# Kernel tuning notes

Measured on AMD Instinct MI355X. Metric: run time of the kernel, lower is better.

Reference implementation:

```python
import jax, jax.numpy as jnp
import numpy as np

HEADS = 16

def _rope(x):
    # x: (B, H, T, D); rotate pairs (even, odd) along last dim, positions along axis 2
    B, H, T, D = x.shape
    half = D // 2
    theta = 10000.0 ** (-jnp.arange(half, dtype=x.dtype) / half)          # (half,)
    angles = jnp.arange(T, dtype=x.dtype)[:, None] * theta                # (T, half)
    sin, cos = jnp.sin(angles), jnp.cos(angles)                           # (T, half)
    x1, x2 = x[..., ::2], x[..., 1::2]                                    # (B,H,T,half)
    rot = jnp.stack([x1 * cos - x2 * sin, x1 * sin + x2 * cos], axis=-1)  # (B,H,T,half,2)
    return rot.reshape(B, H, T, D)

def setup_inputs() -> dict:
    key = jax.random.key(0)
    k1, k2, k3 = jax.random.split(key, 3)
    B, T, C = 2, 2048, 1024
    return {
        "x": jax.random.normal(k1, (B, T, C), dtype=jnp.float32),
        "W_qkv": jax.random.normal(k2, (3 * C, C), dtype=jnp.float32) * 0.02,
        "W_out": jax.random.normal(k3, (C, C), dtype=jnp.float32) * 0.02,
        "window": 256,
    }

def reference(x, W_qkv, W_out, window):
    B, T, C = x.shape
    H = HEADS
    D = C // H
    # fused QKV projection (torch Linear: y = x @ W.T)
    qkv = jnp.einsum('btc,fc->btf', x, W_qkv)            # (B,T,3C)
    qkv = qkv.reshape(B, T, H, 3 * D).transpose(0, 2, 1, 3)  # (B,H,T,3D)
    q, k, v = jnp.split(qkv, 3, axis=-1)                 # each (B,H,T,D)
    q, k = _rope(q), _rope(k)
    # causal + local-window boolean mask: allow j in [i-window, i]
    i = jnp.arange(T)[:, None]
    j = jnp.arange(T)[None, :]
    mask = (j <= i) & (j >= i - window)                  # (T,T) bool
    scale = 1.0 / jnp.sqrt(jnp.asarray(D, dtype=x.dtype))
    scores = jnp.einsum('bhqd,bhkd->bhqk', q, k) * scale # (B,H,T,T)
    scores = jnp.where(mask[None, None], scores, -jnp.inf)
    attn = jax.nn.softmax(scores, axis=-1)
    out = jnp.einsum('bhqk,bhkd->bhqd', attn, v)         # (B,H,T,D)
    out = out.transpose(0, 2, 1, 3).reshape(B, T, C)
    return jnp.einsum('btc,oc->bto', out, W_out)
```

## Files before the change

kernel.cpp:

```cpp
#include <hip/hip_runtime.h>

typedef float f32x4 __attribute__((ext_vector_type(4)));
typedef __bf16 bf16x8 __attribute__((ext_vector_type(8)));
typedef unsigned short u16x4 __attribute__((ext_vector_type(4)));

__device__ __forceinline__ unsigned short f2bf(float f) {
  union { float f; unsigned int u; } v; v.f = f;
  unsigned int r = (v.u + 0x7FFFu + ((v.u >> 16) & 1u)) >> 16;
  return (unsigned short)r;
}
__device__ __forceinline__ float bf2f(unsigned short h) {
  union { unsigned int u; float f; } v; v.u = ((unsigned int)h) << 16;
  return v.f;
}
__device__ __forceinline__ void gload_lds16(const void* g, void* l) {
  __builtin_amdgcn_global_load_lds(
      (const __attribute__((address_space(1))) unsigned int*)g,
      (__attribute__((address_space(3))) unsigned int*)l, 16, 0, 0);
}

__global__ __launch_bounds__(256) void prep_kernel(
    const float* __restrict__ x, const float* __restrict__ wqkv,
    const float* __restrict__ wout, unsigned short* __restrict__ xb,
    unsigned short* __restrict__ wqkvb, unsigned short* __restrict__ woutb,
    float2* __restrict__ tab) {
  const int N1 = 1048576, N2 = 786432, N3 = 262144;
  int idx = blockIdx.x * 256 + threadIdx.x;
  if (idx < N1 + N2 + N3) {
    const float* src; unsigned short* dst; int i = idx;
    if (i < N1)           { src = x;    dst = xb; }
    else if (i < N1 + N2) { i -= N1;      src = wqkv; dst = wqkvb; }
    else                  { i -= N1 + N2; src = wout; dst = woutb; }
    float4 v = ((const float4*)src)[i];
    u16x4 o;
    o.x = f2bf(v.x); o.y = f2bf(v.y); o.z = f2bf(v.z); o.w = f2bf(v.w);
    ((u16x4*)dst)[i] = o;
  } else {
    int i = idx - (N1 + N2 + N3);
    if (i < 65536) {
      int t = i >> 5, p = i & 31;
      float theta = exp2f(-(float)p * 0.4152410118609203f);
      float sn, cs;
      sincosf((float)t * theta, &sn, &cs);
      tab[i] = make_float2(cs, sn);
    }
  }
}

#define G1_SLOT ((128 + 256) * 64)

__global__ __launch_bounds__(512, 1) void gemm1_qkv(
    const unsigned short* __restrict__ A,
    const unsigned short* __restrict__ B,
    unsigned short* __restrict__ Cq,
    const float2* __restrict__ tab) {
  __shared__ unsigned short lds[3 * G1_SLOT];
  const int K = 1024, NJ = 3072, NT = 16;
  const int tid = threadIdx.x;
  const int bm = blockIdx.y * 128, bn = blockIdx.x * 256;
  const int lane = tid & 63, w = tid >> 6, wr = w >> 2, wc = w & 3;
  const int rq = lane & 15, hi = lane >> 4;

  auto stage = [&](int slot, int kt) {
    unsigned short* s = lds + slot * G1_SLOT;
#pragma unroll
    for (int p = 0; p < 2; ++p) {
      int ch = tid + p * 512;
      int row = ch >> 3, blk = (ch & 7) ^ (row & 7);
      gload_lds16(A + (size_t)(bm + row) * K + kt + blk * 8, s + ch * 8);
    }
#pragma unroll
    for (int p = 0; p < 4; ++p) {
      int ch = tid + p * 512;
      int row = ch >> 3, blk = (ch & 7) ^ (row & 7);
      gload_lds16(B + (size_t)(bn + row) * K + kt + blk * 8,
                  s + 128 * 64 + ch * 8);
    }
  };

  f32x4 acc[4][4] = {};
  auto compute = [&](int slot) {
    const unsigned short* sA = lds + slot * G1_SLOT;
    const unsigned short* sB = sA + 128 * 64;
#pragma unroll
    for (int k = 0; k < 2; ++k) {
      bf16x8 fa[4], fb[4];
#pragma unroll
      for (int m = 0; m < 4; ++m) {
        int r = wr * 64 + m * 16 + rq;
        int b = (hi + k * 4) ^ (r & 7);
        fa[m] = *(const bf16x8*)(sA + r * 64 + b * 8);
      }
#pragma unroll
      for (int n = 0; n < 4; ++n) {
        int r = wc * 64 + n * 16 + rq;
        int b = (hi + k * 4) ^ (r & 7);
        fb[n] = *(const bf16x8*)(sB + r * 64 + b * 8);
      }
#pragma unroll
      for (int m = 0; m < 4; ++m)
#pragma unroll
        for (int n = 0; n < 4; ++n)
          acc[m][n] = __builtin_amdgcn_mfma_f32_16x16x32_bf16(fa[m], fb[n], acc[m][n], 0, 0, 0);
    }
  };

  stage(0, 0);
  stage(1, 64);
  for (int t = 0; t < NT; ++t) {
    asm volatile("s_waitcnt lgkmcnt(0)" ::: "memory");
    __builtin_amdgcn_s_barrier();
    if (t + 2 < NT) stage((t + 2) % 3, (t + 2) * 64);
    if (t < NT - 2)
      asm volatile("s_waitcnt vmcnt(12)" ::: "memory");
    else if (t == NT - 2)
      asm volatile("s_waitcnt vmcnt(6)" ::: "memory");
    else
      asm volatile("s_waitcnt vmcnt(0)" ::: "memory");
    __builtin_amdgcn_s_barrier();
    compute(t % 3);
  }

  const int r0 = bm + wr * 64 + hi * 4;
  const int c0 = bn + wc * 64 + rq;
#pragma unroll
  for (int m = 0; m < 4; ++m)
#pragma unroll
    for (int n = 0; n < 4; ++n) {
      int col = c0 + n * 16;
      int cw = col % 192;
      bool dorot = cw < 128;
      int p = (cw & 63) >> 1;
#pragma unroll
      for (int j = 0; j < 4; ++j) {
        int row = r0 + m * 16 + j;
        float val = acc[m][n][j];
        float part = __shfl_xor(val, 1);
        float outv = val;
        if (dorot) {
          float2 cssn = tab[(row & 2047) * 32 + p];
          outv = (col & 1) ? (part * cssn.y + val * cssn.x)
                           : (val * cssn.x - part * cssn.y);
        }
        Cq[(size_t)row * NJ + col] = f2bf(outv);
      }
    }
}

template <bool OUTBF16>
__global__ __launch_bounds__(256) void gemm_bt(const unsigned short* __restrict__ A,
                                               const unsigned short* __restrict__ B,
                                               void* __restrict__ C,
                                               int M, int N, int K) {
  __shared__ unsigned short As[128][32];
  __shared__ unsigned short Bs[128][32];
  const int tid = threadIdx.x;
  const int lane = tid & 63;
  const int w = tid >> 6, wr = w >> 1, wc = w & 1;
  const int bm = blockIdx.y * 128, bn = blockIdx.x * 128;
  const int t4 = tid >> 2, c8 = (tid & 3) * 8;
  const unsigned short* Ab = A + (size_t)(bm + t4) * K + c8;
  const unsigned short* Bb = B + (size_t)(bn + t4) * K + c8;
  const int rq = lane & 15, kg = (lane >> 4) * 8;
  f32x4 acc[4][4] = {};
  for (int kt = 0; kt < K; kt += 32) {
    gload_lds16(Ab + kt,                  &As[t4][c8]);
    gload_lds16(Ab + kt + (size_t)64 * K, &As[t4 + 64][c8]);
    gload_lds16(Bb + kt,                  &Bs[t4][c8]);
    gload_lds16(Bb + kt + (size_t)64 * K, &Bs[t4 + 64][c8]);
    __syncthreads();
    bf16x8 fa[4], fb[4];
#pragma unroll
    for (int m = 0; m < 4; ++m) fa[m] = *(const bf16x8*)&As[wr * 64 + m * 16 + rq][kg];
#pragma unroll
    for (int n = 0; n < 4; ++n) fb[n] = *(const bf16x8*)&Bs[wc * 64 + n * 16 + rq][kg];
#pragma unroll
    for (int m = 0; m < 4; ++m)
#pragma unroll
      for (int n = 0; n < 4; ++n)
        acc[m][n] = __builtin_amdgcn_mfma_f32_16x16x32_bf16(fa[m], fb[n], acc[m][n], 0, 0, 0);
    __syncthreads();
  }
  const int r0 = bm + wr * 64 + (lane >> 4) * 4;
  const int c0 = bn + wc * 64 + rq;
#pragma unroll
  for (int m = 0; m < 4; ++m)
#pragma unroll
    for (int n = 0; n < 4; ++n)
#pragma unroll
      for (int j = 0; j < 4; ++j) {
        int row = r0 + m * 16 + j, col = c0 + n * 16;
        if (OUTBF16)
          ((unsigned short*)C)[(size_t)row * N + col] = f2bf(acc[m][n][j]);
        else
          ((float*)C)[(size_t)row * N + col] = acc[m][n][j];
      }
}

#define WMAX 256
__global__ __launch_bounds__(256) void attn_kernel(const unsigned short* __restrict__ qkv,
                                                   unsigned short* __restrict__ attnb,
                                                   const int* __restrict__ winp) {
  __shared__ unsigned short Qs[64][72];
  __shared__ unsigned short KPs[320 * 72];
  __shared__ unsigned short Vt[64][328];
  const int T = 2048;
  const int tid = threadIdx.x;
  const int bid = blockIdx.x;
  const int qt = bid & 31;
  const int bh = bid >> 5;
  const int b = bh >> 4, h = bh & 15;
  const int qbase = qt * 64;
  const int kbase = qbase - WMAX;
  const int win = *winp;
  const unsigned short* base = qkv + (size_t)b * T * 3072 + h * 192;
  const int tr = tid >> 2, tc = (tid & 3) * 16;
  {
    const unsigned short* s = base + (size_t)(qbase + tr) * 3072 + tc;
    *(int4*)&Qs[tr][tc]     = *(const int4*)s;
    *(int4*)&Qs[tr][tc + 8] = *(const int4*)(s + 8);
  }
#pragma unroll
  for (int p5 = 0; p5 < 5; ++p5) {
    int s = p5 * 64 + tr;
    int j = kbase + s;
    int jc = j < 0 ? 0 : j;
    const unsigned short* sk = base + (size_t)jc * 3072 + 64 + tc;
    *(int4*)&KPs[s * 72 + tc]     = *(const int4*)sk;
    *(int4*)&KPs[s * 72 + tc + 8] = *(const int4*)(sk + 8);
    const unsigned short* sv = base + (size_t)jc * 3072 + 128 + tc;
    unsigned short tmp[16];
    *(int4*)&tmp[0] = *(const int4*)sv;
    *(int4*)&tmp[8] = *(const int4*)(sv + 8);
#pragma unroll
    for (int e = 0; e < 16; ++e) Vt[tc + e][s] = tmp[e];
  }
  __syncthreads();
  const int lane = tid & 63, wv = tid >> 6;
  const int rbase = wv * 16;
  const int rq = lane & 15, kg = (lane >> 4) * 8;
  bf16x8 qa[2];
#pragma unroll
  for (int kk = 0; kk < 2; ++kk)
    qa[kk] = *(const bf16x8*)&Qs[rbase + rq][kk * 32 + kg];
  float sc[20][4];
#pragma unroll
  for (int n = 0; n < 20; ++n) {
    f32x4 s = {};
#pragma unroll
    for (int kk = 0; kk < 2; ++kk) {
      bf16x8 kb = *(const bf16x8*)&KPs[(n * 16 + rq) * 72 + kk * 32 + kg];
      s = __builtin_amdgcn_mfma_f32_16x16x32_bf16(qa[kk], kb, s, 0, 0, 0);
    }
#pragma unroll
    for (int r = 0; r < 4; ++r) sc[n][r] = s[r];
  }
  const float scale = 0.125f;
#pragma unroll
  for (int r = 0; r < 4; ++r) {
    const int i = qbase + rbase + (lane >> 4) * 4 + r;
    float mx = -1e30f;
#pragma unroll
    for (int n = 0; n < 20; ++n) {
      int j = kbase + n * 16 + rq;
      bool valid = (j >= 0) && (j <= i) && (i - j <= win);
      float v = valid ? sc[n][r] * scale : -1e30f;
      sc[n][r] = v;
      mx = fmaxf(mx, v);
    }
#pragma unroll
    for (int off = 1; off < 16; off <<= 1) mx = fmaxf(mx, __shfl_xor(mx, off));
    float sum = 0.f;
#pragma unroll
    for (int n = 0; n < 20; ++n) {
      float pv = __expf(sc[n][r] - mx);
      sc[n][r] = pv;
      sum += pv;
    }
#pragma unroll
    for (int off = 1; off < 16; off <<= 1) sum += __shfl_xor(sum, off);
    float inv = 1.0f / sum;
#pragma unroll
    for (int n = 0; n < 20; ++n) sc[n][r] *= inv;
  }
  __syncthreads();
#pragma unroll
  for (int n = 0; n < 20; ++n)
#pragma unroll
    for (int r = 0; r < 4; ++r)
      KPs[(rbase + (lane >> 4) * 4 + r) * 328 + n * 16 + rq] = f2bf(sc[n][r]);
  f32x4 oacc[4] = {};
#pragma unroll
  for (int kk = 0; kk < 10; ++kk) {
    bf16x8 pa = *(const bf16x8*)&KPs[(rbase + rq) * 328 + kk * 32 + kg];
#pragma unroll
    for (int n = 0; n < 4; ++n) {
      bf16x8 vb = *(const bf16x8*)&Vt[n * 16 + rq][kk * 32 + kg];
      oacc[n] = __builtin_amdgcn_mfma_f32_16x16x32_bf16(pa, vb, oacc[n], 0, 0, 0);
    }
  }
#pragma unroll
  for (int n = 0; n < 4; ++n)
#pragma unroll
    for (int j = 0; j < 4; ++j) {
      int r = qbase + rbase + (lane >> 4) * 4 + j;
      int d = n * 16 + rq;
      attnb[(size_t)(b * T + r) * 1024 + h * 64 + d] = f2bf(oacc[n][j]);
    }
}

extern "C" void kernel_launch(void* const* d_in, const int* in_sizes, int n_in,
                              void* d_out, int out_size, void* d_ws, size_t ws_size,
                              hipStream_t stream) {
  const float* x    = (const float*)d_in[0];
  const float* Wqkv = (const float*)d_in[1];
  const float* Wout = (const float*)d_in[2];
  const int*   winp = (const int*)d_in[3];

  const int M = 4096, C = 1024, N1 = 3072;
  unsigned short* xb    = (unsigned short*)d_ws;
  unsigned short* wqkvb = xb    + (size_t)M * C;
  unsigned short* woutb = wqkvb + (size_t)N1 * C;
  unsigned short* qkvb  = woutb + (size_t)C * C;
  unsigned short* attnb = qkvb  + (size_t)M * N1;
  float2*         tab   = (float2*)(attnb + (size_t)M * C);

  const int PREP = 1048576 + 786432 + 262144 + 65536;
  prep_kernel<<<(PREP + 255) / 256, 256, 0, stream>>>(x, Wqkv, Wout, xb, wqkvb,
                                                      woutb, tab);

  gemm1_qkv<<<dim3(12, 32), 512, 0, stream>>>(xb, wqkvb, qkvb, tab);

  attn_kernel<<<2 * 16 * 32, 256, 0, stream>>>(qkvb, attnb, winp);

  dim3 g2(C / 128, M / 128);
  gemm_bt<false><<<g2, 256, 0, stream>>>(attnb, woutb, (float*)d_out, M, C, C);
}
```

Measured before the change: 214.3 us.

## Simplify QKV GEMM to single-buffered tiles, swizzle V transpose, skip masked score tiles

The QKV projection GEMM drops its 512-thread, triple-buffered 128x256 pipeline and becomes the simpler 256-thread 128x128 single-stage loop, which raises block count but gives up load/compute overlap. The attention kernel now XOR-swizzles columns of the transposed V tile in shared memory to reduce bank conflicts. It also skips QK^T MFMAs for 16-key tiles that lie fully outside the causal range. The output GEMM template is reduced to a float-only version, which is a cleanup.

```diff
diff --git a/kernel.cpp b/kernel.cpp
--- a/kernel.cpp
+++ b/kernel.cpp
@@ -47,80 +47,41 @@
   }
 }
 
-#define G1_SLOT ((128 + 256) * 64)
-
-__global__ __launch_bounds__(512, 1) void gemm1_qkv(
+__global__ __launch_bounds__(256) void gemm1_rope(
     const unsigned short* __restrict__ A,
     const unsigned short* __restrict__ B,
     unsigned short* __restrict__ Cq,
     const float2* __restrict__ tab) {
-  __shared__ unsigned short lds[3 * G1_SLOT];
-  const int K = 1024, NJ = 3072, NT = 16;
+  __shared__ unsigned short As[128][32];
+  __shared__ unsigned short Bs[128][32];
+  const int K = 1024, NJ = 3072;
   const int tid = threadIdx.x;
-  const int bm = blockIdx.y * 128, bn = blockIdx.x * 256;
-  const int lane = tid & 63, w = tid >> 6, wr = w >> 2, wc = w & 3;
-  const int rq = lane & 15, hi = lane >> 4;
-
-  auto stage = [&](int slot, int kt) {
-    unsigned short* s = lds + slot * G1_SLOT;
-#pragma unroll
-    for (int p = 0; p < 2; ++p) {
-      int ch = tid + p * 512;
-      int row = ch >> 3, blk = (ch & 7) ^ (row & 7);
-      gload_lds16(A + (size_t)(bm + row) * K + kt + blk * 8, s + ch * 8);
-    }
-#pragma unroll
-    for (int p = 0; p < 4; ++p) {
-      int ch = tid + p * 512;
-      int row = ch >> 3, blk = (ch & 7) ^ (row & 7);
-      gload_lds16(B + (size_t)(bn + row) * K + kt + blk * 8,
-                  s + 128 * 64 + ch * 8);
-    }
-  };
-
+  const int lane = tid & 63;
+  const int w = tid >> 6, wr = w >> 1, wc = w & 1;
+  const int bm = blockIdx.y * 128, bn = blockIdx.x * 128;
+  const int t4 = tid >> 2, c8 = (tid & 3) * 8;
+  const unsigned short* Ab = A + (size_t)(bm + t4) * K + c8;
+  const unsigned short* Bb = B + (size_t)(bn + t4) * K + c8;
+  const int rq = lane & 15, hi = lane >> 4, kg = hi * 8;
   f32x4 acc[4][4] = {};
-  auto compute = [&](int slot) {
-    const unsigned short* sA = lds + slot * G1_SLOT;
-    const unsigned short* sB = sA + 128 * 64;
-#pragma unroll
-    for (int k = 0; k < 2; ++k) {
-      bf16x8 fa[4], fb[4];
-#pragma unroll
-      for (int m = 0; m < 4; ++m) {
-        int r = wr * 64 + m * 16 + rq;
-        int b = (hi + k * 4) ^ (r & 7);
-        fa[m] = *(const bf16x8*)(sA + r * 64 + b * 8);
-      }
-#pragma unroll
-      for (int n = 0; n < 4; ++n) {
-        int r = wc * 64 + n * 16 + rq;
-        int b = (hi + k * 4) ^ (r & 7);
-        fb[n] = *(const bf16x8*)(sB + r * 64 + b * 8);
-      }
-#pragma unroll
-      for (int m = 0; m < 4; ++m)
-#pragma unroll
-        for (int n = 0; n < 4; ++n)
-          acc[m][n] = __builtin_amdgcn_mfma_f32_16x16x32_bf16(fa[m], fb[n], acc[m][n], 0, 0, 0);
-    }
-  };
-
-  stage(0, 0);
-  stage(1, 64);
-  for (int t = 0; t < NT; ++t) {
-    asm volatile("s_waitcnt lgkmcnt(0)" ::: "memory");
-    __builtin_amdgcn_s_barrier();
-    if (t + 2 < NT) stage((t + 2) % 3, (t + 2) * 64);
-    if (t < NT - 2)
-      asm volatile("s_waitcnt vmcnt(12)" ::: "memory");
-    else if (t == NT - 2)
-      asm volatile("s_waitcnt vmcnt(6)" ::: "memory");
-    else
-      asm volatile("s_waitcnt vmcnt(0)" ::: "memory");
-    __builtin_amdgcn_s_barrier();
-    compute(t % 3);
-  }
-
+  for (int kt = 0; kt < K; kt += 32) {
+    gload_lds16(Ab + kt,                  &As[t4][c8]);
+    gload_lds16(Ab + kt + (size_t)64 * K, &As[t4 + 64][c8]);
+    gload_lds16(Bb + kt,                  &Bs[t4][c8]);
+    gload_lds16(Bb + kt + (size_t)64 * K, &Bs[t4 + 64][c8]);
+    __syncthreads();
+    bf16x8 fa[4], fb[4];
+#pragma unroll
+    for (int m = 0; m < 4; ++m) fa[m] = *(const bf16x8*)&As[wr * 64 + m * 16 + rq][kg];
+#pragma unroll
+    for (int n = 0; n < 4; ++n) fb[n] = *(const bf16x8*)&Bs[wc * 64 + n * 16 + rq][kg];
+#pragma unroll
+    for (int m = 0; m < 4; ++m)
+#pragma unroll
+      for (int n = 0; n < 4; ++n)
+        acc[m][n] = __builtin_amdgcn_mfma_f32_16x16x32_bf16(fa[m], fb[n], acc[m][n], 0, 0, 0);
+    __syncthreads();
+  }
   const int r0 = bm + wr * 64 + hi * 4;
   const int c0 = bn + wc * 64 + rq;
 #pragma unroll
@@ -147,11 +108,10 @@
     }
 }
 
-template <bool OUTBF16>
-__global__ __launch_bounds__(256) void gemm_bt(const unsigned short* __restrict__ A,
-                                               const unsigned short* __restrict__ B,
-                                               void* __restrict__ C,
-                                               int M, int N, int K) {
+__global__ __launch_bounds__(256) void gemm_bt_f32(const unsigned short* __restrict__ A,
+                                                   const unsigned short* __restrict__ B,
+                                                   float* __restrict__ C,
+                                                   int M, int N, int K) {
   __shared__ unsigned short As[128][32];
   __shared__ unsigned short Bs[128][32];
   const int tid = threadIdx.x;
@@ -188,13 +148,8 @@
 #pragma unroll
     for (int n = 0; n < 4; ++n)
 #pragma unroll
-      for (int j = 0; j < 4; ++j) {
-        int row = r0 + m * 16 + j, col = c0 + n * 16;
-        if (OUTBF16)
-          ((unsigned short*)C)[(size_t)row * N + col] = f2bf(acc[m][n][j]);
-        else
-          ((float*)C)[(size_t)row * N + col] = acc[m][n][j];
-      }
+      for (int j = 0; j < 4; ++j)
+        C[(size_t)(r0 + m * 16 + j) * N + c0 + n * 16] = acc[m][n][j];
 }
 
 #define WMAX 256
@@ -215,6 +170,7 @@
   const int win = *winp;
   const unsigned short* base = qkv + (size_t)b * T * 3072 + h * 192;
   const int tr = tid >> 2, tc = (tid & 3) * 16;
+  const int vswz = (tid & 3) << 4;
   {
     const unsigned short* s = base + (size_t)(qbase + tr) * 3072 + tc;
     *(int4*)&Qs[tr][tc]     = *(const int4*)s;
@@ -232,8 +188,9 @@
     unsigned short tmp[16];
     *(int4*)&tmp[0] = *(const int4*)sv;
     *(int4*)&tmp[8] = *(const int4*)(sv + 8);
-#pragma unroll
-    for (int e = 0; e < 16; ++e) Vt[tc + e][s] = tmp[e];
+    int ssw = s ^ vswz;
+#pragma unroll
+    for (int e = 0; e < 16; ++e) Vt[tc + e][ssw] = tmp[e];
   }
   __syncthreads();
   const int lane = tid & 63, wv = tid >> 6;
@@ -246,14 +203,20 @@
   float sc[20][4];
 #pragma unroll
   for (int n = 0; n < 20; ++n) {
-    f32x4 s = {};
-#pragma unroll
-    for (int kk = 0; kk < 2; ++kk) {
-      bf16x8 kb = *(const bf16x8*)&KPs[(n * 16 + rq) * 72 + kk * 32 + kg];
-      s = __builtin_amdgcn_mfma_f32_16x16x32_bf16(qa[kk], kb, s, 0, 0, 0);
-    }
-#pragma unroll
-    for (int r = 0; r < 4; ++r) sc[n][r] = s[r];
+    int jlo = kbase + n * 16;
+    if (jlo + 15 >= 0 && jlo <= qbase + rbase + 15) {
+      f32x4 s = {};
+#pragma unroll
+      for (int kk = 0; kk < 2; ++kk) {
+        bf16x8 kb = *(const bf16x8*)&KPs[(n * 16 + rq) * 72 + kk * 32 + kg];
+        s = __builtin_amdgcn_mfma_f32_16x16x32_bf16(qa[kk], kb, s, 0, 0, 0);
+      }
+#pragma unroll
+      for (int r = 0; r < 4; ++r) sc[n][r] = s[r];
+    } else {
+#pragma unroll
+      for (int r = 0; r < 4; ++r) sc[n][r] = -1e30f;
+    }
   }
   const float scale = 0.125f;
 #pragma unroll
@@ -295,7 +258,7 @@
     bf16x8 pa = *(const bf16x8*)&KPs[(rbase + rq) * 328 + kk * 32 + kg];
 #pragma unroll
     for (int n = 0; n < 4; ++n) {
-      bf16x8 vb = *(const bf16x8*)&Vt[n * 16 + rq][kk * 32 + kg];
+      bf16x8 vb = *(const bf16x8*)&Vt[n * 16 + rq][(kk * 32 + kg) ^ (n << 4)];
       oacc[n] = __builtin_amdgcn_mfma_f32_16x16x32_bf16(pa, vb, oacc[n], 0, 0, 0);
     }
   }
@@ -329,10 +292,10 @@
   prep_kernel<<<(PREP + 255) / 256, 256, 0, stream>>>(x, Wqkv, Wout, xb, wqkvb,
                                                       woutb, tab);
 
-  gemm1_qkv<<<dim3(12, 32), 512, 0, stream>>>(xb, wqkvb, qkvb, tab);
+  gemm1_rope<<<dim3(N1 / 128, M / 128), 256, 0, stream>>>(xb, wqkvb, qkvb, tab);
 
   attn_kernel<<<2 * 16 * 32, 256, 0, stream>>>(qkvb, attnb, winp);
 
-  dim3 g2(C / 128, M / 128);
-  gemm_bt<false><<<g2, 256, 0, stream>>>(attnb, woutb, (float*)d_out, M, C, C);
-}
+  gemm_bt_f32<<<dim3(C / 128, M / 128), 256, 0, stream>>>(attnb, woutb,
+                                                          (float*)d_out, M, C, C);
+}
```

Result: slower. 228.8 us (+6.8%).
